# Performance work log

Measured on AMD Instinct MI355X. Metric: run time of the kernel, lower is better.

## Reference

```python
import jax, jax.numpy as jnp
import numpy as np

GAMMA = 0.2
P = 3
N = 16384


def setup_inputs() -> dict:
    key = jax.random.key(0)
    k1, k2 = jax.random.split(key)
    y_pred = jax.random.normal(k1, (N, 2), dtype=jnp.float32)
    y_true = jax.random.randint(k2, (N,), 0, 2, dtype=jnp.int32)
    return {"y_pred": y_pred, "y_true": y_true}


def reference(y_pred, y_true):
    # softmax over classes, take probability of class 1 -> [N]
    s = jax.nn.softmax(y_pred, axis=-1)[:, 1]
    pos_mask = (y_true == 1)
    neg_mask = ~pos_mask
    # difference[j, i] = pos_i - neg_j - gamma  (rows: negatives, cols: positives)
    diff = s[None, :] - s[:, None] - GAMMA  # [N, N]
    pair = neg_mask[:, None] & pos_mask[None, :]
    valid = pair & (diff < 0.0)
    # sum of (-diff)^p over masked entries == hinge^p penalty
    contrib = jnp.where(valid, (-diff) ** P, jnp.zeros_like(diff))
    return jnp.sum(contrib)
```

## Files before the change

### kernel.cpp

```cpp
#include <hip/hip_runtime.h>
#include <math.h>

#define GAMMA_F 0.2f
#define NT 1024
#define NB 512
#define DLO 0.25f
#define DSCALE (NB / 1.5f)

__device__ __forceinline__ float sig2(float2 y) {
    return 1.0f / (1.0f + __expf(y.x - y.y));
}

__device__ __forceinline__ int bucket_of(float x) {
    int k = (int)floorf((x + DLO) * DSCALE);
    return k < 0 ? 0 : (k >= NB ? NB - 1 : k);
}

extern "C" __global__ __launch_bounds__(NT) void softauc_onepass(
        const float* __restrict__ y_pred, const int* __restrict__ y_true,
        int n, float* __restrict__ out) {
    __shared__ double S[8 * NB];
    __shared__ double4 wtot[NT / 64];
    __shared__ double wred[NT / 64];

    int tid = threadIdx.x, lane = tid & 63, w = tid >> 6;

    for (int i = tid; i < 8 * NB; i += NT) S[i] = 0.0;
    __syncthreads();

    const float2* __restrict__ yp2 = (const float2*)y_pred;
    const int stride4 = NT * 4;
    int nfull = n - (n % stride4);

    for (int base = 0; base < nfull; base += stride4) {
        float2 ya = yp2[base + tid];
        float2 yb = yp2[base + NT + tid];
        float2 yc = yp2[base + 2 * NT + tid];
        float2 yd = yp2[base + 3 * NT + tid];
        int ta = y_true[base + tid];
        int tb = y_true[base + NT + tid];
        int tc = y_true[base + 2 * NT + tid];
        int td = y_true[base + 3 * NT + tid];
        #pragma unroll
        for (int q = 0; q < 4; ++q) {
            float2 y = (q == 0) ? ya : (q == 1) ? yb : (q == 2) ? yc : yd;
            int t = (q == 0) ? ta : (q == 1) ? tb : (q == 2) ? tc : td;
            float s = sig2(y);
            bool isp = (t == 1);
            float x = isp ? s - GAMMA_F : s;
            int off0 = (isp ? 0 : 4 * NB) + bucket_of(x);
            double d = (double)x, d2 = d * d;
            atomicAdd(&S[off0], 1.0);
            atomicAdd(&S[off0 + NB], d);
            atomicAdd(&S[off0 + 2 * NB], d2);
            atomicAdd(&S[off0 + 3 * NB], d2 * d);
        }
    }
    for (int r = nfull + tid; r < n; r += NT) {
        float2 y = yp2[r];
        float s = sig2(y);
        bool isp = (y_true[r] == 1);
        float x = isp ? s - GAMMA_F : s;
        int off0 = (isp ? 0 : 4 * NB) + bucket_of(x);
        double d = (double)x, d2 = d * d;
        atomicAdd(&S[off0], 1.0);
        atomicAdd(&S[off0 + NB], d);
        atomicAdd(&S[off0 + 2 * NB], d2);
        atomicAdd(&S[off0 + 3 * NB], d2 * d);
    }
    __syncthreads();

    int k = (NB - 1) - tid;
    double c0 = 0.0, c1 = 0.0, c2 = 0.0, c3 = 0.0;
    if (tid < NB) {
        c0 = S[4 * NB + k];
        c1 = S[5 * NB + k];
        c2 = S[6 * NB + k];
        c3 = S[7 * NB + k];
    }
    double i0 = c0, i1 = c1, i2 = c2, i3 = c3;
    #pragma unroll
    for (int d = 1; d < 64; d <<= 1) {
        double t0 = __shfl_up(i0, d, 64);
        double t1 = __shfl_up(i1, d, 64);
        double t2 = __shfl_up(i2, d, 64);
        double t3 = __shfl_up(i3, d, 64);
        if (lane >= d) { i0 += t0; i1 += t1; i2 += t2; i3 += t3; }
    }
    if (lane == 63) wtot[w] = make_double4(i0, i1, i2, i3);
    __syncthreads();

    double term = 0.0;
    if (tid < NB) {
        double o0 = 0.0, o1 = 0.0, o2 = 0.0, o3 = 0.0;
        for (int ww = 0; ww < w; ++ww) {
            double4 t = wtot[ww];
            o0 += t.x; o1 += t.y; o2 += t.z; o3 += t.w;
        }
        double e0 = o0 + i0 - c0;
        double e1 = o1 + i1 - c1;
        double e2 = o2 + i2 - c2;
        double e3 = o3 + i3 - c3;
        double P0 = S[k], P1 = S[NB + k], P2 = S[2 * NB + k], P3 = S[3 * NB + k];
        term = e3 * P0 - 3.0 * e2 * P1 + 3.0 * e1 * P2 - e0 * P3;
    }

    #pragma unroll
    for (int off = 32; off > 0; off >>= 1) term += __shfl_down(term, off, 64);
    if (lane == 0) wred[w] = term;
    __syncthreads();
    if (tid == 0) {
        double t = 0.0;
        #pragma unroll
        for (int ww = 0; ww < NT / 64; ++ww) t += wred[ww];
        out[0] = (float)t;
    }
}

extern "C" void kernel_launch(void* const* d_in, const int* in_sizes, int n_in,
                              void* d_out, int out_size, void* d_ws, size_t ws_size,
                              hipStream_t stream) {
    const float* y_pred = (const float*)d_in[0];
    const int* y_true = (const int*)d_in[1];
    int n = in_sizes[1];
    float* out = (float*)d_out;
    (void)n_in; (void)out_size; (void)d_ws; (void)ws_size;

    softauc_onepass<<<dim3(1), dim3(NT), 0, stream>>>(y_pred, y_true, n, out);
}
```

Before: 68.73 us.

## Split histogram into multi-block fixed-point pass plus single-block reduction

Replaces the single-block kernel with two kernels. The first spreads the histogram build over many blocks, each using 64-bit integer fixed-point atomics in shared memory instead of double atomics, and writes per-block partial histograms to workspace. The second sums the partials, converts them back to double, and runs the existing prefix-scan and moment combination. This aims to remove the single-CU serialization and the slow shared-memory double atomics, at the cost of a second launch, a global round trip through 16 partial histograms, and fixed-point rounding error.

```diff
diff --git a/kernel.cpp b/kernel.cpp
--- a/kernel.cpp
+++ b/kernel.cpp
@@ -2,10 +2,14 @@
 #include <math.h>
 
 #define GAMMA_F 0.2f
+#define K1_BS 1024
 #define NT 1024
 #define NB 512
+#define NH (8 * NB)
 #define DLO 0.25f
 #define DSCALE (NB / 1.5f)
+#define SCALE 1.099511627776e12
+#define INV_SCALE (1.0 / 1.099511627776e12)
 
 __device__ __forceinline__ float sig2(float2 y) {
     return 1.0f / (1.0f + __expf(y.x - y.y));
@@ -16,67 +20,57 @@
     return k < 0 ? 0 : (k >= NB ? NB - 1 : k);
 }
 
-extern "C" __global__ __launch_bounds__(NT) void softauc_onepass(
+extern "C" __global__ __launch_bounds__(K1_BS) void k1_hist(
         const float* __restrict__ y_pred, const int* __restrict__ y_true,
-        int n, float* __restrict__ out) {
-    __shared__ double S[8 * NB];
+        int n, unsigned long long* __restrict__ part) {
+    __shared__ unsigned long long H[NH];
+    int tid = threadIdx.x;
+    for (int i = tid; i < NH; i += K1_BS) H[i] = 0ULL;
+    __syncthreads();
+
+    int i = blockIdx.x * K1_BS + tid;
+    if (i < n) {
+        float2 y = ((const float2*)y_pred)[i];
+        float s = sig2(y);
+        bool isp = (y_true[i] == 1);
+        float x = isp ? s - GAMMA_F : s;
+        int off0 = (isp ? 0 : 4 * NB) + bucket_of(x);
+        double d = (double)x, d2 = d * d;
+        atomicAdd(&H[off0],          (unsigned long long)(long long)SCALE);
+        atomicAdd(&H[off0 + NB],     (unsigned long long)(long long)(d * SCALE));
+        atomicAdd(&H[off0 + 2 * NB], (unsigned long long)(long long)(d2 * SCALE));
+        atomicAdd(&H[off0 + 3 * NB], (unsigned long long)(long long)(d2 * d * SCALE));
+    }
+    __syncthreads();
+
+    unsigned long long* dst = part + (size_t)blockIdx.x * NH;
+    for (int j = tid; j < NH; j += K1_BS) dst[j] = H[j];
+}
+
+extern "C" __global__ __launch_bounds__(NT) void k2_reduce(
+        int nblk, const unsigned long long* __restrict__ part,
+        float* __restrict__ out) {
+    __shared__ double H[NH];
     __shared__ double4 wtot[NT / 64];
     __shared__ double wred[NT / 64];
 
     int tid = threadIdx.x, lane = tid & 63, w = tid >> 6;
 
-    for (int i = tid; i < 8 * NB; i += NT) S[i] = 0.0;
-    __syncthreads();
-
-    const float2* __restrict__ yp2 = (const float2*)y_pred;
-    const int stride4 = NT * 4;
-    int nfull = n - (n % stride4);
-
-    for (int base = 0; base < nfull; base += stride4) {
-        float2 ya = yp2[base + tid];
-        float2 yb = yp2[base + NT + tid];
-        float2 yc = yp2[base + 2 * NT + tid];
-        float2 yd = yp2[base + 3 * NT + tid];
-        int ta = y_true[base + tid];
-        int tb = y_true[base + NT + tid];
-        int tc = y_true[base + 2 * NT + tid];
-        int td = y_true[base + 3 * NT + tid];
-        #pragma unroll
-        for (int q = 0; q < 4; ++q) {
-            float2 y = (q == 0) ? ya : (q == 1) ? yb : (q == 2) ? yc : yd;
-            int t = (q == 0) ? ta : (q == 1) ? tb : (q == 2) ? tc : td;
-            float s = sig2(y);
-            bool isp = (t == 1);
-            float x = isp ? s - GAMMA_F : s;
-            int off0 = (isp ? 0 : 4 * NB) + bucket_of(x);
-            double d = (double)x, d2 = d * d;
-            atomicAdd(&S[off0], 1.0);
-            atomicAdd(&S[off0 + NB], d);
-            atomicAdd(&S[off0 + 2 * NB], d2);
-            atomicAdd(&S[off0 + 3 * NB], d2 * d);
-        }
-    }
-    for (int r = nfull + tid; r < n; r += NT) {
-        float2 y = yp2[r];
-        float s = sig2(y);
-        bool isp = (y_true[r] == 1);
-        float x = isp ? s - GAMMA_F : s;
-        int off0 = (isp ? 0 : 4 * NB) + bucket_of(x);
-        double d = (double)x, d2 = d * d;
-        atomicAdd(&S[off0], 1.0);
-        atomicAdd(&S[off0 + NB], d);
-        atomicAdd(&S[off0 + 2 * NB], d2);
-        atomicAdd(&S[off0 + 3 * NB], d2 * d);
+    for (int i = tid; i < NH; i += NT) {
+        unsigned long long s = 0ULL;
+        #pragma unroll 4
+        for (int b = 0; b < nblk; ++b) s += part[(size_t)b * NH + i];
+        H[i] = (double)(long long)s * INV_SCALE;
     }
     __syncthreads();
 
     int k = (NB - 1) - tid;
     double c0 = 0.0, c1 = 0.0, c2 = 0.0, c3 = 0.0;
     if (tid < NB) {
-        c0 = S[4 * NB + k];
-        c1 = S[5 * NB + k];
-        c2 = S[6 * NB + k];
-        c3 = S[7 * NB + k];
+        c0 = H[4 * NB + k];
+        c1 = H[5 * NB + k];
+        c2 = H[6 * NB + k];
+        c3 = H[7 * NB + k];
     }
     double i0 = c0, i1 = c1, i2 = c2, i3 = c3;
     #pragma unroll
@@ -101,7 +95,7 @@
         double e1 = o1 + i1 - c1;
         double e2 = o2 + i2 - c2;
         double e3 = o3 + i3 - c3;
-        double P0 = S[k], P1 = S[NB + k], P2 = S[2 * NB + k], P3 = S[3 * NB + k];
+        double P0 = H[k], P1 = H[NB + k], P2 = H[2 * NB + k], P3 = H[3 * NB + k];
         term = e3 * P0 - 3.0 * e2 * P1 + 3.0 * e1 * P2 - e0 * P3;
     }
 
@@ -124,7 +118,11 @@
     const int* y_true = (const int*)d_in[1];
     int n = in_sizes[1];
     float* out = (float*)d_out;
-    (void)n_in; (void)out_size; (void)d_ws; (void)ws_size;
+    (void)n_in; (void)out_size; (void)ws_size;
 
-    softauc_onepass<<<dim3(1), dim3(NT), 0, stream>>>(y_pred, y_true, n, out);
+    int nblk = (n + K1_BS - 1) / K1_BS;
+    unsigned long long* part = (unsigned long long*)d_ws;
+
+    k1_hist<<<dim3(nblk), dim3(K1_BS), 0, stream>>>(y_pred, y_true, n, part);
+    k2_reduce<<<dim3(1), dim3(NT), 0, stream>>>(nblk, part, out);
 }
```

After: 68.10 us. About the same (-0.9%).
